# Optimization experiments

Measured on AMD Instinct MI355X. Metric: run time of the kernel, lower is better.

The kernel has to match this reference:

```python
import jax, jax.numpy as jnp
import numpy as np

B, T, D, H = 2, 2048, 1024, 16
DH = D // H
PD = 6
_PAIRS = [(0, 1), (0, 2), (0, 3), (1, 2), (1, 3), (2, 3)]
_J6 = jnp.array([[0, 0, 0, 0, 0, 1], [0, 0, 0, 0, -1, 0], [0, 0, 0, 1, 0, 0],
                 [0, 0, 1, 0, 0, 0], [0, -1, 0, 0, 0, 0], [1, 0, 0, 0, 0, 0]], dtype=jnp.float32)


def exterior(p1, p2):
    # Plucker line coordinates of the 2-plane spanned by p1,p2 in R^4, normalized.
    parts = [p1[..., i] * p2[..., j] - p1[..., j] * p2[..., i] for i, j in _PAIRS]
    L = jnp.stack(parts, axis=-1)
    n = jnp.linalg.norm(L, axis=-1, keepdims=True)
    return L / jnp.maximum(n, 1e-12)


def setup_inputs() -> dict:
    key = jax.random.key(0)
    ks = jax.random.split(key, 12)
    s = 0.02
    A = 0.99 * jnp.broadcast_to(jnp.eye(PD, dtype=jnp.float32), (H, PD, PD))
    return {
        'x': jax.random.normal(ks[0], (B, T, D), jnp.float32),
        'Wqkv': jax.random.normal(ks[1], (D, 3 * D), jnp.float32) * s,
        'bqkv': jnp.zeros((3 * D,), jnp.float32),
        'W1w': jax.random.normal(ks[2], (D, 4 * H), jnp.float32) * s,
        'W2w': jax.random.normal(ks[3], (D, 4 * H), jnp.float32) * s,
        'W1r': jax.random.normal(ks[4], (D, 4 * H), jnp.float32) * s,
        'W2r': jax.random.normal(ks[5], (D, 4 * H), jnp.float32) * s,
        'Wmv': jax.random.normal(ks[6], (D, D), jnp.float32) * s,
        'bmv': jnp.zeros((D,), jnp.float32),
        'Wg': jax.random.normal(ks[7], (D, H), jnp.float32) * s,
        'bg': jnp.zeros((H,), jnp.float32),
        'mem_scale': jnp.full((H,), 0.1, jnp.float32),
        'Wout': jax.random.normal(ks[8], (D, D), jnp.float32) * s,
        'bout': jnp.zeros((D,), jnp.float32),
        'A': A,
    }


def reference(x, Wqkv, bqkv, W1w, W2w, W1r, W2r, Wmv, bmv, Wg, bg, mem_scale, Wout, bout, A):
    Bx, Tx, Dx = x.shape
    # ---- causal softmax attention ----
    qkv = (x @ Wqkv + bqkv).reshape(Bx, Tx, 3, H, DH).transpose(2, 0, 3, 1, 4)
    q, k, v = qkv[0], qkv[1], qkv[2]            # (B,H,T,dh)
    scores = jnp.einsum('bhtd,bhsd->bhts', q, k) * (DH ** -0.5)
    mask = jnp.triu(jnp.ones((Tx, Tx), bool), 1)
    scores = jnp.where(mask, -jnp.inf, scores)
    attn = jax.nn.softmax(scores, axis=-1)      # dropout is identity in eval
    seq_out = jnp.einsum('bhts,bhsd->bthd', attn, v).reshape(Bx, Tx, Dx)
    # ---- write/read lines (Plucker) ----
    x_prev = jnp.concatenate([jnp.zeros((Bx, 1, Dx), x.dtype), x[:, :-1]], axis=1)
    w1 = (x_prev @ W1w).reshape(Bx, Tx, H, 4)
    w2 = (x @ W2w).reshape(Bx, Tx, H, 4)
    write_lines = exterior(w1, w2)              # (B,T,H,6)
    r1 = (x @ W1r).reshape(Bx, Tx, H, 4)
    r2 = (x @ W2r).reshape(Bx, Tx, H, 4)
    read_lines = exterior(r1, r2)               # (B,T,H,6)
    Jw = jnp.einsum('bthi,ij->bthj', write_lines, _J6)
    Jw_T = Jw.transpose(1, 0, 2, 3)             # (T,B,H,6)
    rd_T = read_lines.transpose(1, 0, 2, 3)     # (T,B,H,6)
    # ---- Riccati-style state scan: M_t = A M_{t-1} A^T + Jw_t Jw_t^T ----
    def step(M, ts):
        rd_t, Jw_t = ts                          # (B,H,6)
        score = jnp.einsum('bhp,bhpq,bhq->bh', rd_t, M, rd_t)
        M = jnp.einsum('hpq,bhqr,hsr->bhps', A, M, A) + Jw_t[..., :, None] * Jw_t[..., None, :]
        return M, score
    M0 = jnp.zeros((Bx, H, PD, PD), x.dtype)
    _, scores_T = jax.lax.scan(step, M0, (rd_T, Jw_T))   # (T,B,H)
    mem_score_t = scores_T.transpose(1, 0, 2)            # (B,T,H)
    # ---- gated memory readout ----
    mem_val = x @ Wmv + bmv
    gate = jax.nn.sigmoid(x @ Wg + bg)                   # (B,T,H)
    gated = jax.nn.sigmoid(mem_score_t * mem_scale[None, None, :]) * gate
    gated = gated.mean(axis=-1, keepdims=True)           # (B,T,1)
    return (seq_out + gated * mem_val) @ Wout + bout
```

## Files before the change

### kernel.cpp

```cpp
#include <hip/hip_runtime.h>
#include <cstdint>
#include <cstddef>

typedef unsigned short u16;
typedef unsigned int u32;
typedef __attribute__((ext_vector_type(4))) float f32x4;
typedef __attribute__((ext_vector_type(4))) float float4v;
typedef __attribute__((ext_vector_type(8))) short short8;

#define LDC 4368

__device__ __forceinline__ float bf2f(u16 u){ return __uint_as_float(((u32)u) << 16); }
__device__ __forceinline__ u16 f2bf(float f){
  u32 x = __float_as_uint(f);
  x += 0x7FFFu + ((x >> 16) & 1u);
  return (u16)(x >> 16);
}
__device__ __forceinline__ u16 f2bf_rhu(float f){
  return (u16)((__float_as_uint(f) + 0x8000u) >> 16);
}
#if __has_builtin(__builtin_amdgcn_exp2f)
#define EXP2(x) __builtin_amdgcn_exp2f(x)
#else
#define EXP2(x) exp2f(x)
#endif
__device__ __forceinline__ void mfma16(f32x4& d, short8 a, short8 b){
  d = __builtin_amdgcn_mfma_f32_16x16x32_bf16(a, b, d, 0, 0, 0);
}
__device__ __forceinline__ void async_lds16(void* lds, const void* g){
  __builtin_amdgcn_global_load_lds((const __attribute__((address_space(1))) u32*)g,
                                   (__attribute__((address_space(3))) u32*)lds, 16, 0, 0);
}
__device__ __forceinline__ float sigm(float x){ return 1.f / (1.f + __expf(-x)); }
__device__ __forceinline__ void storev(u16* p, float v){ *p = f2bf(v); }
__device__ __forceinline__ void storev(float* p, float v){ *p = v; }

__device__ __forceinline__ void t32(const float* __restrict__ src, u16* __restrict__ dst,
                                    int R, int Ccols, int c0, int r0, int tid, u16 tile[32][33])
{
  int tx = tid & 31, ty0 = tid >> 5;
  #pragma unroll
  for (int i = 0; i < 4; i++){
    int r = r0 + ty0 + i * 8, c = c0 + tx;
    u16 v = 0;
    if (r < R && c < Ccols) v = f2bf(src[(size_t)r * Ccols + c]);
    tile[ty0 + i * 8][tx] = v;
  }
  __syncthreads();
  #pragma unroll
  for (int i = 0; i < 4; i++){
    int cc = c0 + ty0 + i * 8, rr = r0 + tx;
    if (cc < Ccols && rr < R) dst[(size_t)cc * R + rr] = tile[tx][ty0 + i * 8];
  }
}

__global__ __launch_bounds__(256) void prep_kernel(
    const float* __restrict__ x, const float* __restrict__ bqkv, const float* __restrict__ bmv,
    const float* __restrict__ bg, const float* __restrict__ Wqkv,
    const float* __restrict__ W1w, const float* __restrict__ W2w,
    const float* __restrict__ W1r, const float* __restrict__ W2r,
    const float* __restrict__ Wmv, const float* __restrict__ Wout, const float* __restrict__ Wg,
    u16* __restrict__ xb, float* __restrict__ biasfull, u16* __restrict__ BT, u16* __restrict__ WoutT)
{
  __shared__ u16 tile[32][33];
  const int b = blockIdx.x, tid = threadIdx.x;
  if (b < 2048){
    int i = b * 256 + tid;
    float4v a = *(const float4v*)(x + (size_t)i * 8);
    float4v c = *(const float4v*)(x + (size_t)i * 8 + 4);
    short8 o;
    #pragma unroll
    for (int j = 0; j < 4; j++){ o[j] = (short)f2bf(a[j]); o[4 + j] = (short)f2bf(c[j]); }
    *(short8*)(xb + (size_t)i * 8) = o;
  } else if (b < 2066){
    int i = (b - 2048) * 256 + tid;
    if (i < 4368){
      float v;
      if (i < 3072) v = bqkv[i];
      else if (i < 3328) v = 0.f;
      else if (i < 4352) v = bmv[i - 3328];
      else v = bg[i - 4352];
      biasfull[i] = v;
    }
  } else if (b < 5138){
    int local = b - 2066;
    t32(Wqkv, BT, 1024, 3072, (local % 96) * 32, (local / 96) * 32, tid, tile);
  } else if (b < 5394){
    int local = b - 5138;
    int z = local >> 6, rem = local & 63;
    const float* src = (z == 0) ? W1w : (z == 1) ? W2w : (z == 2) ? W1r : W2r;
    t32(src, BT + (size_t)(3072 + z * 64) * 1024, 1024, 64, (rem & 1) * 32, (rem >> 1) * 32, tid, tile);
  } else if (b < 7442){
    int local = b - 5394;
    int z = local >> 10, rem = local & 1023;
    const float* src = z ? Wout : Wmv;
    u16* dst = z ? WoutT : (BT + (size_t)3328 * 1024);
    t32(src, dst, 1024, 1024, (rem & 31) * 32, (rem >> 5) * 32, tid, tile);
  } else {
    int local = b - 7442;
    t32(Wg, BT + (size_t)4352 * 1024, 1024, 16, 0, local * 32, tid, tile);
  }
}

template<typename OT>
__global__ __launch_bounds__(256) void gemm_bt(const u16* __restrict__ Ag, const u16* __restrict__ BTg,
                                               const float* __restrict__ bias, OT* __restrict__ Cg,
                                               int M, int N, int K, int ldc)
{
  __shared__ __align__(16) u16 As[2][128 * 32];
  __shared__ __align__(16) u16 Bs[2][128 * 32];
  const int tid = threadIdx.x, lane = tid & 63, w = tid >> 6;
  const int l15 = lane & 15, l4 = lane >> 4;
  const int qx = gridDim.x >> 3, bid = blockIdx.x;
  const int fid = (bid & 7) * qx + (bid >> 3);
  const int m0 = (fid & 31) * 128, n0 = (fid >> 5) * 128;
  const int wr = w >> 1, wc = w & 1;
  f32x4 acc[4][4] = {};
  const u16* aP[2]; const u16* bP[2];
  #pragma unroll
  for (int j = 0; j < 2; j++){
    int i = w * 128 + j * 64 + lane;
    int lrow = i >> 3, cc = i & 7;
    int sc = cc ^ (lrow & 7);
    int grow = lrow * 2 + (sc >> 2);
    int ka = (sc & 3) * 8;
    aP[j] = Ag + (size_t)(m0 + grow) * K + ka;
    int rb = n0 + grow; if (rb > N - 1) rb = N - 1;
    bP[j] = BTg + (size_t)rb * K + ka;
  }
  const int nk = K >> 5;
  #pragma unroll
  for (int j = 0; j < 2; j++){
    async_lds16((char*)As[0] + w * 2048 + j * 1024, aP[j]);
    async_lds16((char*)Bs[0] + w * 2048 + j * 1024, bP[j]);
  }
  __syncthreads();
  for (int t = 0; t < nk; t++){
    const int cur = t & 1;
    if (t + 1 < nk){
      const int k0 = (t + 1) << 5;
      char* An = (char*)As[cur ^ 1] + w * 2048;
      char* Bn = (char*)Bs[cur ^ 1] + w * 2048;
      #pragma unroll
      for (int j = 0; j < 2; j++){
        async_lds16(An + j * 1024, aP[j] + k0);
        async_lds16(Bn + j * 1024, bP[j] + k0);
      }
    }
    const char* Ab = (const char*)As[cur];
    const char* Bb = (const char*)Bs[cur];
    short8 a[4], b[4];
    #pragma unroll
    for (int mi = 0; mi < 4; mi++){
      int r = wr * 64 + mi * 16 + l15;
      int lrow = r >> 1;
      int slot = (((r & 1) << 2) + l4) ^ (lrow & 7);
      a[mi] = *(const short8*)(Ab + lrow * 128 + slot * 16);
    }
    #pragma unroll
    for (int ni = 0; ni < 4; ni++){
      int r = wc * 64 + ni * 16 + l15;
      int lrow = r >> 1;
      int slot = (((r & 1) << 2) + l4) ^ (lrow & 7);
      b[ni] = *(const short8*)(Bb + lrow * 128 + slot * 16);
    }
    #pragma unroll
    for (int mi = 0; mi < 4; mi++)
      #pragma unroll
      for (int ni = 0; ni < 4; ni++)
        mfma16(acc[mi][ni], a[mi], b[ni]);
    __syncthreads();
  }
  #pragma unroll
  for (int mi = 0; mi < 4; mi++){
    #pragma unroll
    for (int ni = 0; ni < 4; ni++){
      int col = n0 + wc * 64 + ni * 16 + l15;
      if (col < N){
        float bv = bias ? bias[col] : 0.f;
        #pragma unroll
        for (int r = 0; r < 4; r++){
          int row = m0 + wr * 64 + mi * 16 + l4 * 4 + r;
          storev(&Cg[(size_t)row * ldc + col], acc[mi][ni][r] + bv);
        }
      }
    }
  }
}

__device__ __forceinline__ void ext6(float* L, const float* p, const float* q){
  L[0] = p[0]*q[1] - p[1]*q[0];
  L[1] = p[0]*q[2] - p[2]*q[0];
  L[2] = p[0]*q[3] - p[3]*q[0];
  L[3] = p[1]*q[2] - p[2]*q[1];
  L[4] = p[1]*q[3] - p[3]*q[1];
  L[5] = p[2]*q[3] - p[3]*q[2];
  float n = sqrtf(L[0]*L[0]+L[1]*L[1]+L[2]*L[2]+L[3]*L[3]+L[4]*L[4]+L[5]*L[5]);
  float inv = 1.f / fmaxf(n, 1e-12f);
  #pragma unroll
  for (int i = 0; i < 6; i++) L[i] *= inv;
}

__global__ __launch_bounds__(256) void lines_powers_kernel(const u16* __restrict__ C, const float* __restrict__ Ain,
                                                           float* __restrict__ rd, float* __restrict__ Jw,
                                                           float* __restrict__ Gk)
{
  __shared__ float Af[36], Cur[36];
  const int blk = blockIdx.x, tid = threadIdx.x;
  if (blk < 256){
    int idx = blk * 256 + tid;
    int h = idx & 15, t = (idx >> 4) & 2047, b = idx >> 15;
    size_t m = (size_t)b * 2048 + t;
    float w1[4] = {0.f, 0.f, 0.f, 0.f}, w2[4], r1[4], r2[4];
    if (t > 0){
      const u16* p = C + (m - 1) * LDC + 3072 + h * 4;
      #pragma unroll
      for (int i = 0; i < 4; i++) w1[i] = bf2f(p[i]);
    }
    {
      const u16* p = C + m * LDC + 3136 + h * 4;
      #pragma unroll
      for (int i = 0; i < 4; i++) w2[i] = bf2f(p[i]);
      p = C + m * LDC + 3200 + h * 4;
      #pragma unroll
      for (int i = 0; i < 4; i++) r1[i] = bf2f(p[i]);
      p = C + m * LDC + 3264 + h * 4;
      #pragma unroll
      for (int i = 0; i < 4; i++) r2[i] = bf2f(p[i]);
    }
    float L[6], R[6];
    ext6(L, w1, w2);
    ext6(R, r1, r2);
    size_t o = ((size_t)(b * 16 + h) * 2048 + t) * 6;
    #pragma unroll
    for (int i = 0; i < 6; i++) rd[o + i] = R[i];
    Jw[o + 0] =  L[5];
    Jw[o + 1] = -L[4];
    Jw[o + 2] =  L[3];
    Jw[o + 3] =  L[2];
    Jw[o + 4] = -L[1];
    Jw[o + 5] =  L[0];
  } else {
    const int h = blk - 256;
    const int p = tid / 6, q = tid % 6;
    if (tid < 36){
      Af[tid] = Ain[h * 36 + tid];
      float id = (p == q) ? 1.f : 0.f;
      Cur[tid] = id;
      Gk[(size_t)h * 65 * 36 + tid] = id;
    }
    __syncthreads();
    for (int k = 1; k <= 64; k++){
      float v = 0.f;
      if (tid < 36){
        #pragma unroll
        for (int j = 0; j < 6; j++) v += Cur[p * 6 + j] * Af[j * 6 + q];
      }
      __syncthreads();
      if (tid < 36){
        Cur[tid] = v;
        Gk[((size_t)h * 65 + k) * 36 + tid] = v;
      }
      __syncthreads();
    }
  }
}

__global__ __launch_bounds__(256) void chunk_tv_kernel(const float* __restrict__ Jw, const float* __restrict__ Ain,
                                                       float* __restrict__ Sb, const u16* __restrict__ C,
                                                       u16* __restrict__ VT)
{
  __shared__ float Jl[4][384];
  __shared__ float Af[4][36], Ml[4][36], Nl[4][36];
  __shared__ u16 tile[32][33];
  const int blk = blockIdx.x, tid = threadIdx.x;
  if (blk < 256){
    const int g = tid >> 6, lt = tid & 63;
    const int task = blk * 4 + g;
    const int c = task & 31, bh = task >> 5, h = bh & 15;
    const int p = lt / 6, q = lt % 6;
    for (int i = lt; i < 384; i += 64) Jl[g][i] = Jw[((size_t)bh * 2048 + c * 64) * 6 + i];
    if (lt < 36){ Af[g][lt] = Ain[h * 36 + lt]; Ml[g][lt] = 0.f; }
    __syncthreads();
    float arow[6], acol[6];
    if (lt < 36){
      #pragma unroll
      for (int k = 0; k < 6; k++){ arow[k] = Af[g][p * 6 + k]; acol[k] = Af[g][q * 6 + k]; }
    }
    for (int s = 0; s < 64; s++){
      float n = 0.f;
      if (lt < 36){
        #pragma unroll
        for (int k = 0; k < 6; k++) n += arow[k] * Ml[g][k * 6 + q];
        Nl[g][lt] = n;
      }
      __syncthreads();
      if (lt < 36){
        float m = Jl[g][s * 6 + p] * Jl[g][s * 6 + q];
        #pragma unroll
        for (int k = 0; k < 6; k++) m += Nl[g][p * 6 + k] * acol[k];
        Ml[g][lt] = m;
      }
      __syncthreads();
    }
    if (lt < 36) Sb[((size_t)bh * 32 + c) * 36 + lt] = Ml[g][lt];
  } else {
    int local = blk - 256;
    int bh = local >> 7, rem = local & 127;
    int b = bh >> 4, h = bh & 15;
    const u16* src = C + (size_t)b * 2048 * LDC + 2048 + h * 64;
    int c0 = (rem & 1) * 32, r0 = (rem >> 1) * 32;
    int tx = tid & 31, ty0 = tid >> 5;
    #pragma unroll
    for (int i = 0; i < 4; i++)
      tile[ty0 + i * 8][tx] = src[(size_t)(r0 + ty0 + i * 8) * LDC + c0 + tx];
    __syncthreads();
    u16* dstb = VT + (size_t)bh * 64 * 2048;
    #pragma unroll
    for (int i = 0; i < 4; i++)
      dstb[(size_t)(c0 + ty0 + i * 8) * 2048 + r0 + tx] = tile[tx][ty0 + i * 8];
  }
}

__global__ __launch_bounds__(64) void boundary_kernel(const float* __restrict__ Sb, const float* __restrict__ Gk,
                                                      float* __restrict__ Bb)
{
  __shared__ float A64[36], Bl[36], Nl[36];
  const int bh = blockIdx.x, h = bh & 15;
  const int tid = threadIdx.x;
  const int p = tid / 6, q = tid % 6;
  if (tid < 36){ A64[tid] = Gk[((size_t)h * 65 + 64) * 36 + tid]; Bl[tid] = 0.f; }
  __syncthreads();
  float arow[6], acol[6];
  if (tid < 36){
    #pragma unroll
    for (int k = 0; k < 6; k++){ arow[k] = A64[p * 6 + k]; acol[k] = A64[q * 6 + k]; }
  }
  for (int c = 0; c < 32; c++){
    if (tid < 36) Bb[((size_t)bh * 32 + c) * 36 + tid] = Bl[tid];
    float n = 0.f;
    if (tid < 36){
      #pragma unroll
      for (int k = 0; k < 6; k++) n += arow[k] * Bl[k * 6 + q];
    }
    __syncthreads();
    if (tid < 36) Nl[tid] = n;
    __syncthreads();
    if (tid < 36){
      float m = Sb[((size_t)bh * 32 + c) * 36 + tid];
      #pragma unroll
      for (int k = 0; k < 6; k++) m += Nl[p * 6 + k] * acol[k];
      Bl[tid] = m;
    }
    __syncthreads();
  }
}

__global__ __launch_bounds__(256) void attn_score_kernel(const u16* __restrict__ C, const u16* __restrict__ VT,
                                                         u16* __restrict__ seqb,
                                                         const float* __restrict__ rd, const float* __restrict__ Jw,
                                                         const float* __restrict__ Gk, const float* __restrict__ Bb,
                                                         float* __restrict__ score)
{
  __shared__ __align__(16) char smem[40960];
  const int blk = blockIdx.x, tid = threadIdx.x;
  if (blk < 1024){
    char* KsB = smem;
    char* VsB = smem + 16384;
    const int bh = blk & 31, bb = bh >> 4, h = bh & 15;
    const int qblk = 31 - (blk >> 5);
    const int lane = tid & 63, w = tid >> 6;
    const int l15 = lane & 15, l4 = lane >> 4;
    u16* Psw = (u16*)(smem + 32768) + w * 1024;
    const int q0 = qblk * 64 + w * 16;
    const float csc = 0.1803368801f;
    const u16* qb = C + (size_t)(bb * 2048 + q0 + l15) * LDC + h * 64 + l4 * 8;
    short8 qf0 = *(const short8*)qb;
    short8 qf1 = *(const short8*)(qb + 32);
    #pragma unroll
    for (int j = 0; j < 8; j++){
      qf0[j] = (short)f2bf(bf2f((u16)qf0[j]) * csc);
      qf1[j] = (short)f2bf(bf2f((u16)qf1[j]) * csc);
    }
    f32x4 o[4] = {};
    float mrun[4], lsum[4];
    #pragma unroll
    for (int r = 0; r < 4; r++){ mrun[r] = -1e30f; lsum[r] = 0.f; }
    const int nkv = qblk + 1;
    const int rowA = tid >> 3, chA = tid & 7;
    const int swA = chA ^ (rowA & 7);
    const u16* Kg = C + (size_t)(bb * 2048) * LDC + 1024 + h * 64 + chA * 8;
    const u16* Vg = VT + ((size_t)bh * 64 + rowA) * 2048 + chA * 8;
    short8 kr0, kr1, vr0, vr1;
    kr0 = *(const short8*)(Kg + (size_t)rowA * LDC);
    kr1 = *(const short8*)(Kg + (size_t)(rowA + 32) * LDC);
    vr0 = *(const short8*)(Vg);
    vr1 = *(const short8*)(Vg + 32 * 2048);
    *(short8*)(KsB + rowA * 128 + swA * 16)        = kr0;
    *(short8*)(KsB + (rowA + 32) * 128 + swA * 16) = kr1;
    *(short8*)(VsB + rowA * 128 + swA * 16)        = vr0;
    *(short8*)(VsB + (rowA + 32) * 128 + swA * 16) = vr1;
    if (nkv > 1){
      kr0 = *(const short8*)(Kg + (size_t)(64 + rowA) * LDC);
      kr1 = *(const short8*)(Kg + (size_t)(64 + rowA + 32) * LDC);
      vr0 = *(const short8*)(Vg + 64);
      vr1 = *(const short8*)(Vg + 64 + 32 * 2048);
    }
    for (int i = 0; i < nkv; i++){
      const int cur = i & 1;
      __syncthreads();
      if (i + 1 < nkv){
        char* Kd = KsB + (cur ^ 1) * 8192;
        char* Vd = VsB + (cur ^ 1) * 8192;
        *(short8*)(Kd + rowA * 128 + swA * 16)        = kr0;
        *(short8*)(Kd + (rowA + 32) * 128 + swA * 16) = kr1;
        *(short8*)(Vd + rowA * 128 + swA * 16)        = vr0;
        *(short8*)(Vd + (rowA + 32) * 128 + swA * 16) = vr1;
        if (i + 2 < nkv){
          int nx = (i + 2) * 64;
          kr0 = *(const short8*)(Kg + (size_t)(nx + rowA) * LDC);
          kr1 = *(const short8*)(Kg + (size_t)(nx + rowA + 32) * LDC);
          vr0 = *(const short8*)(Vg + nx);
          vr1 = *(const short8*)(Vg + nx + 32 * 2048);
        }
      }
      const char* Ks = KsB + cur * 8192;
      const char* Vs = VsB + cur * 8192;
      const bool diag = (i == qblk);
      f32x4 s4[4] = {};
      __builtin_amdgcn_s_setprio(1);
      #pragma unroll
      for (int j = 0; j < 4; j++){
        const int srow = j * 16 + l15, rm = srow & 7;
        const char* base = Ks + srow * 128;
        short8 b0 = *(const short8*)(base + ((l4 ^ rm) << 4));
        short8 b1 = *(const short8*)(base + (((4 + l4) ^ rm) << 4));
        mfma16(s4[j], qf0, b0);
        mfma16(s4[j], qf1, b1);
      }
      __builtin_amdgcn_s_setprio(0);
      float ps[4][4], lm[4];
      #pragma unroll
      for (int r = 0; r < 4; r++){
        float v0 = s4[0][r], v1 = s4[1][r], v2 = s4[2][r], v3 = s4[3][r];
        if (diag){
          int qrow = w * 16 + l4 * 4 + r;
          if (l15 > qrow)      v0 = -1e30f;
          if (16 + l15 > qrow) v1 = -1e30f;
          if (32 + l15 > qrow) v2 = -1e30f;
          if (48 + l15 > qrow) v3 = -1e30f;
        }
        lm[r] = fmaxf(fmaxf(v0, v1), fmaxf(v2, v3));
        ps[r][0] = v0; ps[r][1] = v1; ps[r][2] = v2; ps[r][3] = v3;
      }
      int ok = (lm[0] <= mrun[0] + 11.5f) && (lm[1] <= mrun[1] + 11.5f)
            && (lm[2] <= mrun[2] + 11.5f) && (lm[3] <= mrun[3] + 11.5f);
      if (!__all(ok)){
        #pragma unroll
        for (int r = 0; r < 4; r++){
          float mx = lm[r];
          mx = fmaxf(mx, __shfl_xor(mx, 1));
          mx = fmaxf(mx, __shfl_xor(mx, 2));
          mx = fmaxf(mx, __shfl_xor(mx, 4));
          mx = fmaxf(mx, __shfl_xor(mx, 8));
          float mnew = fmaxf(mrun[r], mx);
          float sc = EXP2(mrun[r] - mnew);
          mrun[r] = mnew;
          lsum[r] *= sc;
          o[0][r] *= sc; o[1][r] *= sc; o[2][r] *= sc; o[3][r] *= sc;
        }
      }
      #pragma unroll
      for (int r = 0; r < 4; r++){
        float p0 = EXP2(ps[r][0] - mrun[r]);
        float p1 = EXP2(ps[r][1] - mrun[r]);
        float p2 = EXP2(ps[r][2] - mrun[r]);
        float p3 = EXP2(ps[r][3] - mrun[r]);
        lsum[r] += (p0 + p1) + (p2 + p3);
        ps[r][0] = p0; ps[r][1] = p1; ps[r][2] = p2; ps[r][3] = p3;
      }
      char* pw = (char*)Psw;
      const int cb = (l15 & 7) * 2;
      #pragma unroll
      for (int r = 0; r < 4; r++){
        const int prow = l4 * 4 + r, rm = prow & 7;
        char* prb = pw + prow * 128 + cb;
        #pragma unroll
        for (int j = 0; j < 4; j++){
          int cj = (j * 2 + (l15 >> 3)) ^ rm;
          *((u16*)(prb + cj * 16)) = f2bf_rhu(ps[r][j]);
        }
      }
      const int prm = l15 & 7;
      short8 pa0 = *(const short8*)(pw + l15 * 128 + ((l4 ^ prm) << 4));
      short8 pa1 = *(const short8*)(pw + l15 * 128 + (((4 + l4) ^ prm) << 4));
      __builtin_amdgcn_s_setprio(1);
      #pragma unroll
      for (int j = 0; j < 4; j++){
        const int drow = j * 16 + l15, rm = drow & 7;
        const char* vb = Vs + drow * 128;
        short8 b0 = *(const short8*)(vb + ((l4 ^ rm) << 4));
        short8 b1 = *(const short8*)(vb + (((4 + l4) ^ rm) << 4));
        mfma16(o[j], pa0, b0);
        mfma16(o[j], pa1, b1);
      }
      __builtin_amdgcn_s_setprio(0);
    }
    #pragma unroll
    for (int r = 0; r < 4; r++){
      float ls = lsum[r];
      ls += __shfl_xor(ls, 1);
      ls += __shfl_xor(ls, 2);
      ls += __shfl_xor(ls, 4);
      ls += __shfl_xor(ls, 8);
      float inv = 1.f / ls;
      size_t base = (size_t)(bb * 2048 + q0 + l4 * 4 + r) * 1024 + h * 64;
      seqb[base + l15]      = f2bf(o[0][r] * inv);
      seqb[base + 16 + l15] = f2bf(o[1][r] * inv);
      seqb[base + 32 + l15] = f2bf(o[2][r] * inv);
      seqb[base + 48 + l15] = f2bf(o[3][r] * inv);
    }
  } else {
    float* Gl = (float*)smem;
    float* Jl = (float*)(smem + 9216);
    float* Bl = (float*)(smem + 16896);
    const int local = blk - 1024;
    const int tblk = local & 7, bh = local >> 3, h = bh & 15;
    const int t0 = tblk * 256;
    for (int i = tid; i < 64 * 36; i += 256) Gl[i] = Gk[(size_t)h * 65 * 36 + i];
    {
      int base = t0 * 6 - 384;
      for (int i = tid; i < 1920; i += 256){
        int s6 = base + i;
        Jl[i] = (s6 >= 0) ? Jw[(size_t)bh * (2048 * 6) + s6] : 0.f;
      }
    }
    for (int i = tid; i < 144; i += 256) Bl[i] = Bb[((size_t)bh * 32 + tblk * 4) * 36 + i];
    __syncthreads();
    float Ar[36];
    #pragma unroll
    for (int i = 0; i < 36; i++) Ar[i] = Gl[36 + i];
    const int t = t0 + tid;
    const int cl = tid >> 6;
    const int dlt = tid & 63;
    float rdv[6];
    {
      const float* rp = rd + ((size_t)bh * 2048 + t) * 6;
      #pragma unroll
      for (int q = 0; q < 6; q++) rdv[q] = rp[q];
    }
    const float* g = Gl + dlt * 36;
    float u[6];
    #pragma unroll
    for (int p = 0; p < 6; p++){
      float s = 0.f;
      #pragma unroll
      for (int q = 0; q < 6; q++) s += rdv[q] * g[q * 6 + p];
      u[p] = s;
    }
    float acc = 0.f;
    #pragma unroll
    for (int p = 0; p < 6; p++){
      float bv = 0.f;
      #pragma unroll
      for (int q = 0; q < 6; q++) bv += Bl[cl * 36 + p * 6 + q] * u[q];
      acc += u[p] * bv;
    }
    float wv[6];
    #pragma unroll
    for (int q = 0; q < 6; q++) wv[q] = rdv[q];
    const int sIdx = tid + 63;
    for (int k = 0; k < dlt; k++){
      const float* jp = Jl + (sIdx - k) * 6;
      float uu = wv[0]*jp[0] + wv[1]*jp[1] + wv[2]*jp[2] + wv[3]*jp[3] + wv[4]*jp[4] + wv[5]*jp[5];
      acc += uu * uu;
      float nw[6];
      #pragma unroll
      for (int q = 0; q < 6; q++)
        nw[q] = wv[0]*Ar[q] + wv[1]*Ar[6+q] + wv[2]*Ar[12+q] + wv[3]*Ar[18+q] + wv[4]*Ar[24+q] + wv[5]*Ar[30+q];
      #pragma unroll
      for (int q = 0; q < 6; q++) wv[q] = nw[q];
    }
    score[(size_t)bh * 2048 + t] = acc;
  }
}

__global__ __launch_bounds__(256) void gated_combine_kernel(const float* __restrict__ score, const u16* __restrict__ C,
                                                            const float* __restrict__ mem_scale,
                                                            const u16* __restrict__ seqb, u16* __restrict__ preb)
{
  __shared__ float gsh[2];
  const int blk = blockIdx.x, tid = threadIdx.x;
  const int m0 = blk * 2;
  if (tid < 2){
    int m = m0 + tid;
    int b = m >> 11, t = m & 2047;
    float acc = 0.f;
    for (int h2 = 0; h2 < 16; h2++){
      float sc = score[(size_t)(b * 16 + h2) * 2048 + t];
      float ms = mem_scale[h2];
      float gp = bf2f(C[(size_t)m * LDC + 4352 + h2]);
      acc += sigm(sc * ms) * sigm(gp);
    }
    gsh[tid] = acc * (1.f / 16.f);
  }
  __syncthreads();
  const int m = m0 + (tid >> 7), d8 = (tid & 127) * 8;
  const float g = gsh[tid >> 7];
  short8 sv = *(const short8*)(seqb + (size_t)m * 1024 + d8);
  short8 mv = *(const short8*)(C + (size_t)m * LDC + 3328 + d8);
  short8 ov;
  #pragma unroll
  for (int j = 0; j < 8; j++){
    float f = bf2f((u16)sv[j]) + g * bf2f((u16)mv[j]);
    ov[j] = (short)f2bf(f);
  }
  *(short8*)(preb + (size_t)m * 1024 + d8) = ov;
}

extern "C" void kernel_launch(void* const* d_in, const int* in_sizes, int n_in,
                              void* d_out, int out_size, void* d_ws, size_t ws_size,
                              hipStream_t stream)
{
  (void)in_sizes; (void)n_in; (void)out_size; (void)ws_size;
  const float* x     = (const float*)d_in[0];
  const float* Wqkv  = (const float*)d_in[1];
  const float* bqkv  = (const float*)d_in[2];
  const float* W1w   = (const float*)d_in[3];
  const float* W2w   = (const float*)d_in[4];
  const float* W1r   = (const float*)d_in[5];
  const float* W2r   = (const float*)d_in[6];
  const float* Wmv   = (const float*)d_in[7];
  const float* bmv   = (const float*)d_in[8];
  const float* Wg    = (const float*)d_in[9];
  const float* bg    = (const float*)d_in[10];
  const float* mem_scale = (const float*)d_in[11];
  const float* Wout  = (const float*)d_in[12];
  const float* bout  = (const float*)d_in[13];
  const float* Am    = (const float*)d_in[14];
  float* out = (float*)d_out;

  char* p = (char*)d_ws;
  auto carve = [&](size_t bytes) -> void* {
    void* r = (void*)p;
    p += (bytes + 255) & ~(size_t)255;
    return r;
  };
  u16*   xb       = (u16*)  carve((size_t)4096 * 1024 * 2);
  u16*   C        = (u16*)  carve((size_t)4096 * LDC * 2);
  u16*   BT       = (u16*)  carve((size_t)LDC * 1024 * 2);
  u16*   WoutT    = (u16*)  carve((size_t)1024 * 1024 * 2);
  float* biasfull = (float*)carve((size_t)LDC * 4);
  u16*   VTb      = (u16*)  carve((size_t)32 * 64 * 2048 * 2);
  u16*   seqb     = (u16*)  carve((size_t)4096 * 1024 * 2);
  float* rdb      = (float*)carve((size_t)32 * 2048 * 6 * 4);
  float* Jwb      = (float*)carve((size_t)32 * 2048 * 6 * 4);
  float* Gk       = (float*)carve((size_t)16 * 65 * 36 * 4);
  float* Sbb      = (float*)carve((size_t)32 * 32 * 36 * 4);
  float* Bbb      = (float*)carve((size_t)32 * 32 * 36 * 4);
  float* scoreb   = (float*)carve((size_t)32 * 2048 * 4);
  u16*   preb     = (u16*)  carve((size_t)4096 * 1024 * 2);

  prep_kernel<<<7474, 256, 0, stream>>>(x, bqkv, bmv, bg, Wqkv, W1w, W2w, W1r, W2r,
                                        Wmv, Wout, Wg, xb, biasfull, BT, WoutT);

  gemm_bt<u16><<<1120, 256, 0, stream>>>(xb, BT, biasfull, C, 4096, LDC, 1024, LDC);

  lines_powers_kernel<<<272, 256, 0, stream>>>(C, Am, rdb, Jwb, Gk);
  chunk_tv_kernel<<<4352, 256, 0, stream>>>(Jwb, Am, Sbb, C, VTb);
  boundary_kernel<<<32, 64, 0, stream>>>(Sbb, Gk, Bbb);
  attn_score_kernel<<<1280, 256, 0, stream>>>(C, VTb, seqb, rdb, Jwb, Gk, Bbb, scoreb);
  gated_combine_kernel<<<2048, 256, 0, stream>>>(scoreb, C, mem_scale, seqb, preb);

  gemm_bt<float><<<256, 256, 0, stream>>>(preb, WoutT, bout, out, 4096, 1024, 1024, 1024);
}
```

Baseline: 198.4 us.

## Fuse line computation into chunk scan and fold boundary scan into score blocks

Line computation (exterior products) now happens inside the chunk-scan kernel. Each 64-thread group computes its chunk's Jw directly into shared memory instead of reloading it from global memory. The serial boundary-state kernel is removed. Each score block redundantly recomputes the chunk-boundary recurrence up to its own chunk from Sb, which cuts two kernel launches and one round trip through global memory. The cost is a serial loop of up to 32 steps with barriers inside each of the 256 score blocks, which may lengthen the tail of the attention kernel.

```diff
diff --git a/kernel.cpp b/kernel.cpp
--- a/kernel.cpp
+++ b/kernel.cpp
@@ -201,50 +201,80 @@
   for (int i = 0; i < 6; i++) L[i] *= inv;
 }
 
-__global__ __launch_bounds__(256) void lines_powers_kernel(const u16* __restrict__ C, const float* __restrict__ Ain,
-                                                           float* __restrict__ rd, float* __restrict__ Jw,
-                                                           float* __restrict__ Gk)
+__global__ __launch_bounds__(256) void chunk_tv_kernel(const u16* __restrict__ C, const float* __restrict__ Ain,
+                                                       float* __restrict__ Sb, u16* __restrict__ VT,
+                                                       float* __restrict__ rd, float* __restrict__ Jw,
+                                                       float* __restrict__ Gk)
 {
-  __shared__ float Af[36], Cur[36];
+  __shared__ float Jl[4][384];
+  __shared__ float Af[4][36], Ml[4][36], Nl[4][36];
+  __shared__ u16 tile[32][33];
+  __shared__ float Pw[36], Cur[36];
   const int blk = blockIdx.x, tid = threadIdx.x;
   if (blk < 256){
-    int idx = blk * 256 + tid;
-    int h = idx & 15, t = (idx >> 4) & 2047, b = idx >> 15;
-    size_t m = (size_t)b * 2048 + t;
-    float w1[4] = {0.f, 0.f, 0.f, 0.f}, w2[4], r1[4], r2[4];
-    if (t > 0){
-      const u16* p = C + (m - 1) * LDC + 3072 + h * 4;
-      #pragma unroll
-      for (int i = 0; i < 4; i++) w1[i] = bf2f(p[i]);
-    }
+    const int g = tid >> 6, lt = tid & 63;
+    const int task = blk * 4 + g;
+    const int c = task & 31, bh = task >> 5, h = bh & 15, b = bh >> 4;
     {
-      const u16* p = C + m * LDC + 3136 + h * 4;
-      #pragma unroll
-      for (int i = 0; i < 4; i++) w2[i] = bf2f(p[i]);
-      p = C + m * LDC + 3200 + h * 4;
-      #pragma unroll
-      for (int i = 0; i < 4; i++) r1[i] = bf2f(p[i]);
-      p = C + m * LDC + 3264 + h * 4;
-      #pragma unroll
-      for (int i = 0; i < 4; i++) r2[i] = bf2f(p[i]);
-    }
-    float L[6], R[6];
-    ext6(L, w1, w2);
-    ext6(R, r1, r2);
-    size_t o = ((size_t)(b * 16 + h) * 2048 + t) * 6;
-    #pragma unroll
-    for (int i = 0; i < 6; i++) rd[o + i] = R[i];
-    Jw[o + 0] =  L[5];
-    Jw[o + 1] = -L[4];
-    Jw[o + 2] =  L[3];
-    Jw[o + 3] =  L[2];
-    Jw[o + 4] = -L[1];
-    Jw[o + 5] =  L[0];
-  } else {
+      const int t = c * 64 + lt;
+      size_t m = (size_t)b * 2048 + t;
+      float w1[4] = {0.f, 0.f, 0.f, 0.f}, w2[4], r1[4], r2[4];
+      if (t > 0){
+        const u16* p2 = C + (m - 1) * LDC + 3072 + h * 4;
+        #pragma unroll
+        for (int i = 0; i < 4; i++) w1[i] = bf2f(p2[i]);
+      }
+      {
+        const u16* p2 = C + m * LDC + 3136 + h * 4;
+        #pragma unroll
+        for (int i = 0; i < 4; i++) w2[i] = bf2f(p2[i]);
+        p2 = C + m * LDC + 3200 + h * 4;
+        #pragma unroll
+        for (int i = 0; i < 4; i++) r1[i] = bf2f(p2[i]);
+        p2 = C + m * LDC + 3264 + h * 4;
+        #pragma unroll
+        for (int i = 0; i < 4; i++) r2[i] = bf2f(p2[i]);
+      }
+      float L[6], R[6];
+      ext6(L, w1, w2);
+      ext6(R, r1, r2);
+      size_t o = ((size_t)bh * 2048 + t) * 6;
+      #pragma unroll
+      for (int i = 0; i < 6; i++) rd[o + i] = R[i];
+      float jv[6] = { L[5], -L[4], L[3], L[2], -L[1], L[0] };
+      #pragma unroll
+      for (int i = 0; i < 6; i++){ Jw[o + i] = jv[i]; Jl[g][lt * 6 + i] = jv[i]; }
+    }
+    const int p = lt / 6, q = lt % 6;
+    if (lt < 36){ Af[g][lt] = Ain[h * 36 + lt]; Ml[g][lt] = 0.f; }
+    __syncthreads();
+    float arow[6], acol[6];
+    if (lt < 36){
+      #pragma unroll
+      for (int k = 0; k < 6; k++){ arow[k] = Af[g][p * 6 + k]; acol[k] = Af[g][q * 6 + k]; }
+    }
+    for (int s = 0; s < 64; s++){
+      float n = 0.f;
+      if (lt < 36){
+        #pragma unroll
+        for (int k = 0; k < 6; k++) n += arow[k] * Ml[g][k * 6 + q];
+        Nl[g][lt] = n;
+      }
+      __syncthreads();
+      if (lt < 36){
+        float m = Jl[g][s * 6 + p] * Jl[g][s * 6 + q];
+        #pragma unroll
+        for (int k = 0; k < 6; k++) m += Nl[g][p * 6 + k] * acol[k];
+        Ml[g][lt] = m;
+      }
+      __syncthreads();
+    }
+    if (lt < 36) Sb[((size_t)bh * 32 + c) * 36 + lt] = Ml[g][lt];
+  } else if (blk < 272){
     const int h = blk - 256;
     const int p = tid / 6, q = tid % 6;
     if (tid < 36){
-      Af[tid] = Ain[h * 36 + tid];
+      Pw[tid] = Ain[h * 36 + tid];
       float id = (p == q) ? 1.f : 0.f;
       Cur[tid] = id;
       Gk[(size_t)h * 65 * 36 + tid] = id;
@@ -254,7 +284,7 @@
       float v = 0.f;
       if (tid < 36){
         #pragma unroll
-        for (int j = 0; j < 6; j++) v += Cur[p * 6 + j] * Af[j * 6 + q];
+        for (int j = 0; j < 6; j++) v += Cur[p * 6 + j] * Pw[j * 6 + q];
       }
       __syncthreads();
       if (tid < 36){
@@ -263,49 +293,8 @@
       }
       __syncthreads();
     }
-  }
-}
-
-__global__ __launch_bounds__(256) void chunk_tv_kernel(const float* __restrict__ Jw, const float* __restrict__ Ain,
-                                                       float* __restrict__ Sb, const u16* __restrict__ C,
-                                                       u16* __restrict__ VT)
-{
-  __shared__ float Jl[4][384];
-  __shared__ float Af[4][36], Ml[4][36], Nl[4][36];
-  __shared__ u16 tile[32][33];
-  const int blk = blockIdx.x, tid = threadIdx.x;
-  if (blk < 256){
-    const int g = tid >> 6, lt = tid & 63;
-    const int task = blk * 4 + g;
-    const int c = task & 31, bh = task >> 5, h = bh & 15;
-    const int p = lt / 6, q = lt % 6;
-    for (int i = lt; i < 384; i += 64) Jl[g][i] = Jw[((size_t)bh * 2048 + c * 64) * 6 + i];
-    if (lt < 36){ Af[g][lt] = Ain[h * 36 + lt]; Ml[g][lt] = 0.f; }
-    __syncthreads();
-    float arow[6], acol[6];
-    if (lt < 36){
-      #pragma unroll
-      for (int k = 0; k < 6; k++){ arow[k] = Af[g][p * 6 + k]; acol[k] = Af[g][q * 6 + k]; }
-    }
-    for (int s = 0; s < 64; s++){
-      float n = 0.f;
-      if (lt < 36){
-        #pragma unroll
-        for (int k = 0; k < 6; k++) n += arow[k] * Ml[g][k * 6 + q];
-        Nl[g][lt] = n;
-      }
-      __syncthreads();
-      if (lt < 36){
-        float m = Jl[g][s * 6 + p] * Jl[g][s * 6 + q];
-        #pragma unroll
-        for (int k = 0; k < 6; k++) m += Nl[g][p * 6 + k] * acol[k];
-        Ml[g][lt] = m;
-      }
-      __syncthreads();
-    }
-    if (lt < 36) Sb[((size_t)bh * 32 + c) * 36 + lt] = Ml[g][lt];
   } else {
-    int local = blk - 256;
+    int local = blk - 272;
     int bh = local >> 7, rem = local & 127;
     int b = bh >> 4, h = bh & 15;
     const u16* src = C + (size_t)b * 2048 * LDC + 2048 + h * 64;
@@ -322,44 +311,10 @@
   }
 }
 
-__global__ __launch_bounds__(64) void boundary_kernel(const float* __restrict__ Sb, const float* __restrict__ Gk,
-                                                      float* __restrict__ Bb)
-{
-  __shared__ float A64[36], Bl[36], Nl[36];
-  const int bh = blockIdx.x, h = bh & 15;
-  const int tid = threadIdx.x;
-  const int p = tid / 6, q = tid % 6;
-  if (tid < 36){ A64[tid] = Gk[((size_t)h * 65 + 64) * 36 + tid]; Bl[tid] = 0.f; }
-  __syncthreads();
-  float arow[6], acol[6];
-  if (tid < 36){
-    #pragma unroll
-    for (int k = 0; k < 6; k++){ arow[k] = A64[p * 6 + k]; acol[k] = A64[q * 6 + k]; }
-  }
-  for (int c = 0; c < 32; c++){
-    if (tid < 36) Bb[((size_t)bh * 32 + c) * 36 + tid] = Bl[tid];
-    float n = 0.f;
-    if (tid < 36){
-      #pragma unroll
-      for (int k = 0; k < 6; k++) n += arow[k] * Bl[k * 6 + q];
-    }
-    __syncthreads();
-    if (tid < 36) Nl[tid] = n;
-    __syncthreads();
-    if (tid < 36){
-      float m = Sb[((size_t)bh * 32 + c) * 36 + tid];
-      #pragma unroll
-      for (int k = 0; k < 6; k++) m += Nl[p * 6 + k] * acol[k];
-      Bl[tid] = m;
-    }
-    __syncthreads();
-  }
-}
-
 __global__ __launch_bounds__(256) void attn_score_kernel(const u16* __restrict__ C, const u16* __restrict__ VT,
                                                          u16* __restrict__ seqb,
                                                          const float* __restrict__ rd, const float* __restrict__ Jw,
-                                                         const float* __restrict__ Gk, const float* __restrict__ Bb,
+                                                         const float* __restrict__ Gk, const float* __restrict__ Sb,
                                                          float* __restrict__ score)
 {
   __shared__ __align__(16) char smem[40960];
@@ -521,9 +476,12 @@
       seqb[base + 48 + l15] = f2bf(o[3][r] * inv);
     }
   } else {
-    float* Gl = (float*)smem;
-    float* Jl = (float*)(smem + 9216);
-    float* Bl = (float*)(smem + 16896);
+    float* Gl  = (float*)smem;
+    float* Jl  = (float*)(smem + 9216);
+    float* Bl  = (float*)(smem + 16896);
+    float* A64s= (float*)(smem + 17472);
+    float* Bw  = (float*)(smem + 17664);
+    float* Nw  = (float*)(smem + 17856);
     const int local = blk - 1024;
     const int tblk = local & 7, bh = local >> 3, h = bh & 15;
     const int t0 = tblk * 256;
@@ -535,7 +493,35 @@
         Jl[i] = (s6 >= 0) ? Jw[(size_t)bh * (2048 * 6) + s6] : 0.f;
       }
     }
-    for (int i = tid; i < 144; i += 256) Bl[i] = Bb[((size_t)bh * 32 + tblk * 4) * 36 + i];
+    {
+      const int p = tid / 6, q = tid % 6;
+      if (tid < 36){ A64s[tid] = Gk[((size_t)h * 65 + 64) * 36 + tid]; Bw[tid] = 0.f; }
+      __syncthreads();
+      float arow[6], acol[6];
+      if (tid < 36){
+        #pragma unroll
+        for (int k = 0; k < 6; k++){ arow[k] = A64s[p * 6 + k]; acol[k] = A64s[q * 6 + k]; }
+      }
+      const int cEnd = tblk * 4;
+      for (int c = 0; c < cEnd + 4; c++){
+        if (tid < 36 && c >= cEnd) Bl[(c - cEnd) * 36 + tid] = Bw[tid];
+        float n = 0.f;
+        if (tid < 36){
+          #pragma unroll
+          for (int k = 0; k < 6; k++) n += arow[k] * Bw[k * 6 + q];
+        }
+        __syncthreads();
+        if (tid < 36) Nw[tid] = n;
+        __syncthreads();
+        if (tid < 36){
+          float m = Sb[((size_t)bh * 32 + c) * 36 + tid];
+          #pragma unroll
+          for (int k = 0; k < 6; k++) m += Nw[p * 6 + k] * acol[k];
+          Bw[tid] = m;
+        }
+        __syncthreads();
+      }
+    }
     __syncthreads();
     float Ar[36];
     #pragma unroll
@@ -657,7 +643,6 @@
   float* Jwb      = (float*)carve((size_t)32 * 2048 * 6 * 4);
   float* Gk       = (float*)carve((size_t)16 * 65 * 36 * 4);
   float* Sbb      = (float*)carve((size_t)32 * 32 * 36 * 4);
-  float* Bbb      = (float*)carve((size_t)32 * 32 * 36 * 4);
   float* scoreb   = (float*)carve((size_t)32 * 2048 * 4);
   u16*   preb     = (u16*)  carve((size_t)4096 * 1024 * 2);
 
@@ -666,10 +651,10 @@
 
   gemm_bt<u16><<<1120, 256, 0, stream>>>(xb, BT, biasfull, C, 4096, LDC, 1024, LDC);
 
-  lines_powers_kernel<<<272, 256, 0, stream>>>(C, Am, rdb, Jwb, Gk);
-  chunk_tv_kernel<<<4352, 256, 0, stream>>>(Jwb, Am, Sbb, C, VTb);
-  boundary_kernel<<<32, 64, 0, stream>>>(Sbb, Gk, Bbb);
-  attn_score_kernel<<<1280, 256, 0, stream>>>(C, VTb, seqb, rdb, Jwb, Gk, Bbb, scoreb);
+  chunk_tv_kernel<<<4368, 256, 0, stream>>>(C, Am, Sbb, VTb, rdb, Jwb, Gk);
+
+  attn_score_kernel<<<1280, 256, 0, stream>>>(C, VTb, seqb, rdb, Jwb, Gk, Sbb, scoreb);
+
   gated_combine_kernel<<<2048, 256, 0, stream>>>(scoreb, C, mem_scale, seqb, preb);
 
   gemm_bt<float><<<256, 256, 0, stream>>>(preb, WoutT, bout, out, 4096, 1024, 1024, 1024);
```

Result: faster. 185.0 us (-6.8%).
